# Kernel optimization log

Hardware: AMD Instinct MI355X
Metric: run time of the kernel (lower is better)

The kernel has to match this reference:

```python
import jax, jax.numpy as jnp
import numpy as np

IOU_THRESHOLD = 0.5
OBJ_WEIGHT = 0.5


def setup_inputs() -> dict:
    key = jax.random.key(0)
    k0, k1, k2, k3, k4 = jax.random.split(key, 5)
    b, t, a = 64, 60, 3
    det0 = jax.random.normal(k0, (b, a, 160, 160, 5), jnp.float32)
    det1 = jax.random.normal(k1, (b, a, 80, 80, 5), jnp.float32)
    det2 = jax.random.normal(k2, (b, a, 40, 40, 5), jnp.float32)
    # scaled anchors in grid-cell units, (s=3 scales, a=3 anchors, wh)
    anchors = jax.random.uniform(k3, (3, a, 2), jnp.float32, 1.0, 10.0)
    # normalized target boxes (x, y, w, h) in [0, 1)
    targets = jax.random.uniform(k4, (b, t, 4), jnp.float32)
    return {"det0": det0, "det1": det1, "det2": det2, "anchors": anchors, "targets": targets}


def _calc_overlap(anchors, zt):
    # anchors: (s, a, 2); zt: (b, t, s, 4) -> iou-like overlap (b, t, s, a)
    s, a = anchors.shape[:2]
    b, t = zt.shape[:2]
    anc = anchors.reshape(1, 1, s, a, 2)
    tg = zt.reshape(b, t, s, 1, 4)
    lb = jnp.maximum(-anc / 2, tg[..., 0:2] - tg[..., 2:4] / 2)
    ub = jnp.minimum(anc / 2, tg[..., 0:2] + tg[..., 2:4] / 2)
    m = jnp.prod((lb < ub).astype(anc.dtype), axis=4)
    inter = jnp.prod(ub - lb, axis=4) * m
    anc_area = jnp.prod(anc, axis=4)                       # (1,1,s,a)
    tgt_area = (tg[..., 2] - tg[..., 0]) * (tg[..., 3] - tg[..., 1])  # (b,t,s,1), faithful to source
    return inter / (anc_area + tgt_area - inter)


def _suppress(overlap, thr):
    # faithful to the sequential in-place edits in suppress_anchors
    b, t, s, a = overlap.shape
    ov = overlap.reshape(b * t, s * a)
    mx = jnp.max(ov, axis=1, keepdims=True)
    ov = jnp.where(ov == mx, 1.0, ov)
    ov = jnp.where(ov < thr, 0.0, ov)
    ov = jnp.where((ov != 0.0) & (ov != 1.0), -1.0, ov)
    return ov.reshape(b, t, s, a)


def _object_loss(det0, det1, det2, anchors, targets):
    preds = [det0, det1, det2]
    b, t = targets.shape[:2]
    s, a = anchors.shape[:2]
    shapes = np.array([(p.shape[2], p.shape[3]) for p in preds])  # (s, 2) static (h, w)
    shapes_f = jnp.asarray(shapes, dtype=targets.dtype)

    mask_flat = jnp.all(targets[..., 0:4] != -1, axis=2).reshape(-1)  # (b*t,)

    # target cells: (cy, cx) = floor((ty, tx) * (h, w)) per scale -> (b, t, s, 2)
    yx = jnp.stack([targets[..., 1], targets[..., 0]], axis=-1)  # (b, t, 2)
    cells = (yx[:, :, None, :] * shapes_f[None, None, :, :]).astype(jnp.int32)

    # zeroed targets: scale by (w, h, w, h), center offsets in [-0.5, 0.5)
    whwh = shapes_f[:, jnp.array([1, 0, 1, 0])]  # (s, 4)
    zt = targets[..., 0:4][:, :, None, :] * whwh[None, None, :, :]  # (b, t, s, 4)
    xy = zt[..., 0:2] - (jnp.floor(zt[..., 0:2]) + 0.5)
    zt = jnp.concatenate([xy, zt[..., 2:4]], axis=-1)

    gt_values = _suppress(_calc_overlap(anchors, zt), IOU_THRESHOLD)  # (b, t, s, a)

    bidx = jnp.repeat(jnp.arange(b, dtype=jnp.int32), t)  # (b*t,)
    aidx = jnp.arange(a, dtype=jnp.int32)[None, :]        # (1, a)

    gt_flat = []
    for si, p in enumerate(preds):
        h, w = int(shapes[si, 0]), int(shapes[si, 1])
        cy = cells[:, :, si, 0].reshape(-1)
        cx = cells[:, :, si, 1].reshape(-1)
        cy = jnp.where(mask_flat, cy, h)  # invalid targets -> out of range -> dropped
        vals = gt_values[:, :, si, :].reshape(-1, a)  # (b*t, a)
        gt = jnp.zeros((b, a, h, w), dtype=targets.dtype)
        gt = gt.at[bidx[:, None], aidx, cy[:, None], cx[:, None]].set(vals, mode='drop')
        gt_flat.append(gt.reshape(-1))

    ground_truth = jnp.concatenate(gt_flat, axis=0)
    logits = jnp.concatenate([p[..., 4].reshape(-1) for p in preds], axis=0)

    # BCEWithLogitsLoss with pos_weight pw: (1-y)*x + (1 + (pw-1)*y) * softplus(-x), mean
    y = ground_truth
    x = logits
    loss = jnp.mean((1.0 - y) * x + (1.0 + (OBJ_WEIGHT - 1.0) * y) * jax.nn.softplus(-x))
    return loss


def reference(det0, det1, det2, anchors, targets):
    return _object_loss(det0, det1, det2, anchors, targets)
```

## Files before the change

kernel.cpp:

```cpp
#include <hip/hip_runtime.h>
#include <math.h>

#define B 64
#define T 60
#define NA 3
#define NS 3
#define BT (B*T)

#define NB0 1600
#define NB1 400
#define NB2 100
#define NB_SCAN (NB0 + NB1 + NB2)
#define NB_CORR ((BT + 255) / 256)
#define NB_ALL (NB_SCAN + NB_CORR)
#define POOL0 (NB0 * 256)
#define POOL1 (NB1 * 256)
#define POOL2 (NB2 * 256)
#define N_TOTAL 6451200.0f

__device__ __forceinline__ float softplus_f(float x) {
    float e = __expf(-fabsf(x));
    return fmaxf(x, 0.0f) + __logf(1.0f + e);
}

__device__ __forceinline__ float pick(float4 f, int ph) {
    return (ph == 1) ? f.x : (ph == 2) ? f.y : (ph == 3) ? f.z : f.w;
}

__device__ __forceinline__ float block_reduce_sum(float v) {
    for (int o = 32; o > 0; o >>= 1) v += __shfl_down(v, o, 64);
    __shared__ float s[4];
    int lane = threadIdx.x & 63;
    int w = threadIdx.x >> 6;
    if (lane == 0) s[w] = v;
    __syncthreads();
    if (threadIdx.x == 0) {
        float t = 0.0f;
        #pragma unroll
        for (int i = 0; i < 4; ++i) t += s[i];
        return t;
    }
    return 0.0f;
}

__device__ __forceinline__ float scan15(const float4* __restrict__ p,
                                        int g0, int stride) {
    float acc = 0.0f;
    int phase = g0 % 5;
    if (phase) {
        #pragma unroll
        for (int grp = 0; grp < 3; ++grp) {
            int base = g0 + (5 * grp) * stride;
            float4 f0 = p[base];
            float4 f1 = p[base + stride];
            float4 f2 = p[base + 2 * stride];
            float4 f3 = p[base + 3 * stride];
            float4 f4 = p[base + 4 * stride];
            acc += softplus_f(pick(f0, phase));
            acc += softplus_f(pick(f1, phase));
            acc += softplus_f(pick(f2, phase));
            acc += softplus_f(pick(f3, phase));
            acc += softplus_f(pick(f4, phase));
        }
    }
    return acc;
}

__global__ void __launch_bounds__(256, 8) fused_main_kernel(
    const float* __restrict__ d0f, const float* __restrict__ d1f,
    const float* __restrict__ d2f, const float* __restrict__ anchors,
    const float* __restrict__ targets, float* __restrict__ partials) {
    float acc = 0.0f;

    if (blockIdx.x < NB0) {
        int g0 = blockIdx.x * 256 + threadIdx.x;
        acc = scan15((const float4*)d0f, g0, POOL0);
    } else if (blockIdx.x < NB0 + NB1) {
        int g0 = (blockIdx.x - NB0) * 256 + threadIdx.x;
        acc = scan15((const float4*)d1f, g0, POOL1);
    } else if (blockIdx.x < NB_SCAN) {
        int g0 = (blockIdx.x - NB0 - NB1) * 256 + threadIdx.x;
        acc = scan15((const float4*)d2f, g0, POOL2);
    } else {
        int tid = (blockIdx.x - NB_SCAN) * 256 + threadIdx.x;
        if (tid < BT) {
            int bi = tid / T;
            const float* tg = targets + tid * 4;
            float tx = tg[0], ty = tg[1], tw = tg[2], th = tg[3];
            bool mask = (tx != -1.0f) && (ty != -1.0f) &&
                        (tw != -1.0f) && (th != -1.0f);
            const int dims[NS] = {160, 80, 40};
            const float* dets[NS] = {d0f, d1f, d2f};

            float ov[NS][NA];
            float mx = -INFINITY;
            #pragma unroll
            for (int si = 0; si < NS; ++si) {
                float D = (float)dims[si];
                float ztx = tx * D, zty = ty * D, ztw = tw * D, zth = th * D;
                float fx = ztx - (floorf(ztx) + 0.5f);
                float fy = zty - (floorf(zty) + 0.5f);
                float tarea = (ztw - fx) * (zth - fy);
                #pragma unroll
                for (int ai = 0; ai < NA; ++ai) {
                    float a0 = anchors[(si * NA + ai) * 2 + 0];
                    float a1 = anchors[(si * NA + ai) * 2 + 1];
                    float lb0 = fmaxf(-0.5f * a0, fx - 0.5f * ztw);
                    float ub0 = fminf( 0.5f * a0, fx + 0.5f * ztw);
                    float lb1 = fmaxf(-0.5f * a1, fy - 0.5f * zth);
                    float ub1 = fminf( 0.5f * a1, fy + 0.5f * zth);
                    float m = ((lb0 < ub0) && (lb1 < ub1)) ? 1.0f : 0.0f;
                    float inter = (ub0 - lb0) * (ub1 - lb1) * m;
                    float v = inter / (a0 * a1 + tarea - inter);
                    ov[si][ai] = v;
                    mx = fmaxf(mx, v);
                }
            }
            if (mask) {
                #pragma unroll
                for (int si = 0; si < NS; ++si) {
                    int D = dims[si];
                    int cy = (int)(ty * (float)D);
                    int cx = (int)(tx * (float)D);
                    if (cy >= 0 && cy < D && cx >= 0 && cx < D) {
                        #pragma unroll
                        for (int ai = 0; ai < NA; ++ai) {
                            float v = ov[si][ai];
                            float y = (v == mx) ? 1.0f
                                    : ((v < 0.5f) ? 0.0f : -1.0f);
                            if (y != 0.0f) {
                                long idx = ((((long)bi * NA + ai) * D + cy) * D + cx) * 5 + 4;
                                float x = dets[si][idx];
                                acc += -y * x - 0.5f * y * softplus_f(-x);
                            }
                        }
                    }
                }
            }
        }
    }

    float bs = block_reduce_sum(acc);
    if (threadIdx.x == 0) partials[blockIdx.x] = bs;
}

__global__ void __launch_bounds__(256) final_kernel(
    const float* __restrict__ wsf, float* __restrict__ out) {
    float acc = 0.0f;
    for (int i = threadIdx.x; i < NB_ALL; i += blockDim.x)
        acc += wsf[i];
    float bs = block_reduce_sum(acc);
    if (threadIdx.x == 0) out[0] = bs / N_TOTAL;
}

extern "C" void kernel_launch(void* const* d_in, const int* in_sizes, int n_in,
                              void* d_out, int out_size, void* d_ws, size_t ws_size,
                              hipStream_t stream) {
    const float* det0    = (const float*)d_in[0];
    const float* det1    = (const float*)d_in[1];
    const float* det2    = (const float*)d_in[2];
    const float* anchors = (const float*)d_in[3];
    const float* targets = (const float*)d_in[4];
    float* out = (float*)d_out;
    float* wsf = (float*)d_ws;

    fused_main_kernel<<<NB_ALL, 256, 0, stream>>>(det0, det1, det2,
                                                  anchors, targets, wsf);
    final_kernel<<<1, 256, 0, stream>>>(wsf, out);
}
```

Measured before the change: 30.85 us.

## Treat three detection tensors as one concatenated stream with nontemporal float4 loads

Replaces the per-tensor scan blocks (1600/400/100 blocks with separate strides) with a uniform 2048-block grid that walks a virtual concatenation of det0, det1 and det2. Each thread issues 15 or 16 strided float4 loads and selects the source tensor per chunk. All loads now use nontemporal hints to avoid polluting cache on a single-pass stream. The aim is to even out per-block work and reduce block count, at the cost of per-load branch/select logic and a trailing partial-load pass.

```diff
diff --git a/kernel.cpp b/kernel.cpp
--- a/kernel.cpp
+++ b/kernel.cpp
@@ -7,24 +7,27 @@
 #define NS 3
 #define BT (B*T)
 
-#define NB0 1600
-#define NB1 400
-#define NB2 100
-#define NB_SCAN (NB0 + NB1 + NB2)
+#define NB_SCAN 2048
 #define NB_CORR ((BT + 255) / 256)
 #define NB_ALL (NB_SCAN + NB_CORR)
-#define POOL0 (NB0 * 256)
-#define POOL1 (NB1 * 256)
-#define POOL2 (NB2 * 256)
+#define NT 524288
 #define N_TOTAL 6451200.0f
+
+#define CH_B1 24000u
+#define CH_B2 30000u
+#define OFF_D1 6144000
+#define OFF_D2 7680000
+#define NB_16TH 780
+
+typedef float float4n __attribute__((ext_vector_type(4)));
 
 __device__ __forceinline__ float softplus_f(float x) {
     float e = __expf(-fabsf(x));
     return fmaxf(x, 0.0f) + __logf(1.0f + e);
 }
 
-__device__ __forceinline__ float pick(float4 f, int ph) {
-    return (ph == 1) ? f.x : (ph == 2) ? f.y : (ph == 3) ? f.z : f.w;
+__device__ __forceinline__ float pickn(float4n f, int ph) {
+    return (ph == 1) ? f[0] : (ph == 2) ? f[1] : (ph == 3) ? f[2] : f[3];
 }
 
 __device__ __forceinline__ float block_reduce_sum(float v) {
@@ -43,44 +46,47 @@
     return 0.0f;
 }
 
-__device__ __forceinline__ float scan15(const float4* __restrict__ p,
-                                        int g0, int stride) {
-    float acc = 0.0f;
-    int phase = g0 % 5;
-    if (phase) {
-        #pragma unroll
-        for (int grp = 0; grp < 3; ++grp) {
-            int base = g0 + (5 * grp) * stride;
-            float4 f0 = p[base];
-            float4 f1 = p[base + stride];
-            float4 f2 = p[base + 2 * stride];
-            float4 f3 = p[base + 3 * stride];
-            float4 f4 = p[base + 4 * stride];
-            acc += softplus_f(pick(f0, phase));
-            acc += softplus_f(pick(f1, phase));
-            acc += softplus_f(pick(f2, phase));
-            acc += softplus_f(pick(f3, phase));
-            acc += softplus_f(pick(f4, phase));
-        }
-    }
-    return acc;
-}
-
 __global__ void __launch_bounds__(256, 8) fused_main_kernel(
     const float* __restrict__ d0f, const float* __restrict__ d1f,
     const float* __restrict__ d2f, const float* __restrict__ anchors,
     const float* __restrict__ targets, float* __restrict__ partials) {
     float acc = 0.0f;
 
-    if (blockIdx.x < NB0) {
+    if (blockIdx.x < NB_SCAN) {
         int g0 = blockIdx.x * 256 + threadIdx.x;
-        acc = scan15((const float4*)d0f, g0, POOL0);
-    } else if (blockIdx.x < NB0 + NB1) {
-        int g0 = (blockIdx.x - NB0) * 256 + threadIdx.x;
-        acc = scan15((const float4*)d1f, g0, POOL1);
-    } else if (blockIdx.x < NB_SCAN) {
-        int g0 = (blockIdx.x - NB0 - NB1) * 256 + threadIdx.x;
-        acc = scan15((const float4*)d2f, g0, POOL2);
+        int p0 = g0 % 5;
+        #pragma unroll
+        for (int grp = 0; grp < 3; ++grp) {
+            float4n f0, f1, f2, f3, f4;
+            #define LOADJ(J, DEST)                                           \
+            {                                                                \
+                const int k = grp * 5 + (J);                                 \
+                const int idx = g0 + k * NT;                                 \
+                const unsigned chunk = blockIdx.x + (unsigned)k * 2048u;     \
+                const float* bp = (chunk < CH_B1) ? d0f                      \
+                                : (chunk < CH_B2) ? d1f : d2f;               \
+                const int off = (chunk < CH_B1) ? idx                        \
+                              : (chunk < CH_B2) ? (idx - OFF_D1)             \
+                                                : (idx - OFF_D2);            \
+                DEST = __builtin_nontemporal_load((const float4n*)bp + off); \
+            }
+            LOADJ(0, f0) LOADJ(1, f1) LOADJ(2, f2) LOADJ(3, f3) LOADJ(4, f4)
+            #undef LOADJ
+            #define EATJ(J, SRC)                                             \
+            {                                                                \
+                const int c = (3 * (grp * 5 + (J))) % 5;                     \
+                int ph = p0 + c; if (ph >= 5) ph -= 5;                       \
+                if (ph) acc += softplus_f(pickn(SRC, ph));                   \
+            }
+            EATJ(0, f0) EATJ(1, f1) EATJ(2, f2) EATJ(3, f3) EATJ(4, f4)
+            #undef EATJ
+        }
+        if (blockIdx.x < NB_16TH) {
+            int idx = g0 + 15 * NT;
+            float4n f = __builtin_nontemporal_load(
+                (const float4n*)d2f + (idx - OFF_D2));
+            if (p0) acc += softplus_f(pickn(f, p0));
+        }
     } else {
         int tid = (blockIdx.x - NB_SCAN) * 256 + threadIdx.x;
         if (tid < BT) {
```

Result: faster. 28.77 us (-6.7%).
